# Kernel optimization log

Hardware: AMD Instinct MI355X
Metric: run time of the kernel (lower is better)

Reference implementation:

```python
import jax, jax.numpy as jnp
import numpy as np

S, B, HID = 2048, 1, 2048
NH, HD = 16, 128  # heads, head_dim (kv_channels); NH*HD == HID
EPS = 1e-5


def setup_inputs() -> dict:
    key = jax.random.key(0)
    ks = jax.random.split(key, 5)
    sc_h = 1.0 / np.sqrt(HID)
    return {
        "hidden_states": jax.random.normal(ks[0], (S, B, HID), jnp.float32),
        "ln_weight": jnp.ones((HID,), jnp.float32),
        "ln_bias": jnp.zeros((HID,), jnp.float32),
        "qkv_weight": jax.random.normal(ks[1], (3 * HID, HID), jnp.float32) * sc_h,
        "qkv_bias": jax.random.normal(ks[2], (3 * HID,), jnp.float32) * 0.02,
        "proj_weight": jax.random.normal(ks[3], (HID, HID), jnp.float32) * sc_h,
        "proj_bias": jax.random.normal(ks[4], (HID,), jnp.float32) * 0.02,
    }


def reference(hidden_states, ln_weight, ln_bias, qkv_weight, qkv_bias, proj_weight, proj_bias):
    s, b, hid = hidden_states.shape
    # LayerNormLinear: LN over last dim, then fused QKV projection
    mu = jnp.mean(hidden_states, axis=-1, keepdims=True)
    var = jnp.mean(jnp.square(hidden_states - mu), axis=-1, keepdims=True)
    ln_x = (hidden_states - mu) * jax.lax.rsqrt(var + EPS) * ln_weight + ln_bias
    mixed = jnp.einsum('sbh,oh->sbo', ln_x, qkv_weight) + qkv_bias  # [S,B,3*HID]
    # fuse_qkv_params=False -> non-interleaved: reshape to [S,B,3*NH,HD], split on dim -2
    mixed = mixed.reshape(s, b, 3 * NH, HD)
    q, k, v = jnp.split(mixed, 3, axis=2)  # each [S,B,NH,HD]
    # scaled dot-product attention with causal mask
    scale = 1.0 / np.sqrt(HD)
    scores = jnp.einsum('sbhd,tbhd->bhst', q, k) * scale  # [B,NH,S,S]
    causal = jnp.tril(jnp.ones((s, s), bool))
    scores = jnp.where(causal, scores, -jnp.inf)
    probs = jax.nn.softmax(scores, axis=-1)
    ctx = jnp.einsum('bhst,tbhd->sbhd', probs, v).reshape(s, b, hid)
    # output projection
    out = jnp.einsum('sbh,oh->sbo', ctx, proj_weight) + proj_bias
    return out
```

## Files before the change

### kernel.cpp

```cpp
#include <hip/hip_runtime.h>
#include <stdint.h>

#define S_LEN 2048
#define HID   2048
#define NHEAD 16
#define HDIM  128
#define LDQK  4096

typedef unsigned short ushort_t;
using bf16x8 = __attribute__((ext_vector_type(8))) short;
using f32x4  = __attribute__((ext_vector_type(4))) float;

__device__ __forceinline__ float bf2f(ushort_t u) {
  union { uint32_t i; float f; } v; v.i = ((uint32_t)u) << 16; return v.f;
}
__device__ __forceinline__ ushort_t f2bf(float f) {
  union { float f; uint32_t i; } v; v.f = f;
  uint32_t r = v.i + 0x7fffu + ((v.i >> 16) & 1u);
  return (ushort_t)(r >> 16);
}
__device__ __forceinline__ void store_val(ushort_t* C, size_t idx, float v) { C[idx] = f2bf(v); }
__device__ __forceinline__ void store_val(float* C, size_t idx, float v) { C[idx] = v; }

__device__ __forceinline__ bf16x8 load8(const ushort_t* p) { return *(const bf16x8*)p; }
__device__ __forceinline__ bf16x8 load8(const float* p) {
  float4 a = *(const float4*)p, b = *(const float4*)(p + 4);
  ushort_t o[8] = { f2bf(a.x), f2bf(a.y), f2bf(a.z), f2bf(a.w),
                    f2bf(b.x), f2bf(b.y), f2bf(b.z), f2bf(b.w) };
  return *(const bf16x8*)o;
}

__device__ __forceinline__ void gl_lds16(const ushort_t* g, short* l) {
  __builtin_amdgcn_global_load_lds((const __attribute__((address_space(1))) void*)g,
                                   (__attribute__((address_space(3))) void*)l, 16, 0, 0);
}

__global__ __launch_bounds__(256) void ln_cvt_fused(const float* __restrict__ x,
                                                    const float* __restrict__ w,
                                                    const float* __restrict__ bln,
                                                    ushort_t* __restrict__ y,
                                                    const float* __restrict__ s1,
                                                    ushort_t* __restrict__ d1, int n1,
                                                    const float* __restrict__ s2,
                                                    ushort_t* __restrict__ d2, int n2) {
  const int t = threadIdx.x;
  if ((int)blockIdx.x >= S_LEN) {
    int i = ((int)blockIdx.x - S_LEN) * 256 + t;
    const float* src; ushort_t* dst;
    if (i < n1) { src = s1; dst = d1; }
    else { i -= n1; if (i >= n2) return; src = s2; dst = d2; }
    float4 a = ((const float4*)src)[i * 2], c = ((const float4*)src)[i * 2 + 1];
    ushort_t o[8] = { f2bf(a.x), f2bf(a.y), f2bf(a.z), f2bf(a.w),
                      f2bf(c.x), f2bf(c.y), f2bf(c.z), f2bf(c.w) };
    ((uint4*)dst)[i] = *(const uint4*)o;
    return;
  }
  const int row = blockIdx.x;
  const float4* xr = (const float4*)(x + (size_t)row * HID);
  float4 v0 = xr[t], v1 = xr[t + 256];
  float s  = v0.x + v0.y + v0.z + v0.w + v1.x + v1.y + v1.z + v1.w;
  float ss = v0.x*v0.x + v0.y*v0.y + v0.z*v0.z + v0.w*v0.w
           + v1.x*v1.x + v1.y*v1.y + v1.z*v1.z + v1.w*v1.w;
#pragma unroll
  for (int off = 32; off > 0; off >>= 1) { s += __shfl_xor(s, off, 64); ss += __shfl_xor(ss, off, 64); }
  __shared__ float red[8];
  const int wv = t >> 6;
  if ((t & 63) == 0) { red[wv * 2] = s; red[wv * 2 + 1] = ss; }
  __syncthreads();
  s  = red[0] + red[2] + red[4] + red[6];
  ss = red[1] + red[3] + red[5] + red[7];
  const float mu   = s * (1.f / HID);
  const float var  = ss * (1.f / HID) - mu * mu;
  const float rstd = rsqrtf(var + 1e-5f);
  const float4* wr = (const float4*)w;
  const float4* br = (const float4*)bln;
  float4 w0 = wr[t], w1 = wr[t + 256];
  float4 b0 = br[t], b1 = br[t + 256];
  ushort_t* yr = y + (size_t)row * HID;
  ushort_t o0[4] = { f2bf((v0.x - mu) * rstd * w0.x + b0.x), f2bf((v0.y - mu) * rstd * w0.y + b0.y),
                     f2bf((v0.z - mu) * rstd * w0.z + b0.z), f2bf((v0.w - mu) * rstd * w0.w + b0.w) };
  ushort_t o1[4] = { f2bf((v1.x - mu) * rstd * w1.x + b1.x), f2bf((v1.y - mu) * rstd * w1.y + b1.y),
                     f2bf((v1.z - mu) * rstd * w1.z + b1.z), f2bf((v1.w - mu) * rstd * w1.w + b1.w) };
  *(uint2*)(&yr[4 * t])         = *(const uint2*)o0;
  *(uint2*)(&yr[4 * (t + 256)]) = *(const uint2*)o1;
}

__global__ __launch_bounds__(256) void ln_kernel(const float* __restrict__ x,
                                                 const float* __restrict__ w,
                                                 const float* __restrict__ b,
                                                 ushort_t* __restrict__ y) {
  const int row = blockIdx.x;
  const int t = threadIdx.x;
  const float4* xr = (const float4*)(x + (size_t)row * HID);
  float4 v0 = xr[t], v1 = xr[t + 256];
  float s  = v0.x + v0.y + v0.z + v0.w + v1.x + v1.y + v1.z + v1.w;
  float ss = v0.x*v0.x + v0.y*v0.y + v0.z*v0.z + v0.w*v0.w
           + v1.x*v1.x + v1.y*v1.y + v1.z*v1.z + v1.w*v1.w;
#pragma unroll
  for (int off = 32; off > 0; off >>= 1) { s += __shfl_xor(s, off, 64); ss += __shfl_xor(ss, off, 64); }
  __shared__ float red[8];
  const int wv = t >> 6;
  if ((t & 63) == 0) { red[wv * 2] = s; red[wv * 2 + 1] = ss; }
  __syncthreads();
  s  = red[0] + red[2] + red[4] + red[6];
  ss = red[1] + red[3] + red[5] + red[7];
  const float mu   = s * (1.f / HID);
  const float var  = ss * (1.f / HID) - mu * mu;
  const float rstd = rsqrtf(var + 1e-5f);
  const float4* wr = (const float4*)w;
  const float4* br = (const float4*)b;
  float4 w0 = wr[t], w1 = wr[t + 256];
  float4 b0 = br[t], b1 = br[t + 256];
  ushort_t* yr = y + (size_t)row * HID;
  ushort_t o0[4] = { f2bf((v0.x - mu) * rstd * w0.x + b0.x), f2bf((v0.y - mu) * rstd * w0.y + b0.y),
                     f2bf((v0.z - mu) * rstd * w0.z + b0.z), f2bf((v0.w - mu) * rstd * w0.w + b0.w) };
  ushort_t o1[4] = { f2bf((v1.x - mu) * rstd * w1.x + b1.x), f2bf((v1.y - mu) * rstd * w1.y + b1.y),
                     f2bf((v1.z - mu) * rstd * w1.z + b1.z), f2bf((v1.w - mu) * rstd * w1.w + b1.w) };
  *(uint2*)(&yr[4 * t])         = *(const uint2*)o0;
  *(uint2*)(&yr[4 * (t + 256)]) = *(const uint2*)o1;
}

template <int MT, bool SPLIT, typename OUT_T>
__global__ __launch_bounds__(256, 3) void gemm_lds(const ushort_t* __restrict__ A,
                                                   const ushort_t* __restrict__ B,
                                                   const float* __restrict__ bias,
                                                   OUT_T* __restrict__ C,
                                                   ushort_t* __restrict__ VTg,
                                                   int M, int N, int K, int ldc) {
  constexpr int MI = MT / 32;
  __shared__ __align__(16) short As[2][MT * 32];
  __shared__ __align__(16) short Bs[2][128 * 32];
  const int mb = blockIdx.x * MT, nb = blockIdx.y * 128;
  const int t = threadIdx.x, wave = t >> 6, lane = t & 63;
  const int wm = (wave >> 1) * (MT / 2), wn = (wave & 1) * 64;
  const int lrow = lane & 15, quad = lane >> 4;
  const int srow = lane >> 2, scol = (lane & 3) * 8;
  const f32x4 vzero = {0.f, 0.f, 0.f, 0.f};

  f32x4 acc[MI][4];
#pragma unroll
  for (int i = 0; i < MI; i++)
#pragma unroll
    for (int j = 0; j < 4; j++) acc[i][j] = vzero;

  auto stage = [&](int k0, int buf) {
#pragma unroll
    for (int kb = 0; kb < MT / 64; kb++) {
      const int c = wave * (MT / 64) + kb;
      gl_lds16(&A[(size_t)(mb + c * 16 + srow) * K + k0 + scol], &As[buf][c * 512]);
    }
#pragma unroll
    for (int kb = 0; kb < 2; kb++) {
      const int c = wave * 2 + kb;
      gl_lds16(&B[(size_t)(nb + c * 16 + srow) * K + k0 + scol], &Bs[buf][c * 512]);
    }
  };

  stage(0, 0);
  int cur = 0;
  for (int k0 = 0; k0 < K; k0 += 32) {
    __syncthreads();
    if (k0 + 32 < K) stage(k0 + 32, cur ^ 1);
    bf16x8 af[MI], bfg[4];
#pragma unroll
    for (int mi = 0; mi < MI; mi++) af[mi] = *(const bf16x8*)(&As[cur][(wm + mi * 16 + lrow) * 32 + quad * 8]);
#pragma unroll
    for (int ni = 0; ni < 4; ni++) bfg[ni] = *(const bf16x8*)(&Bs[cur][(wn + ni * 16 + lrow) * 32 + quad * 8]);
#pragma unroll
    for (int mi = 0; mi < MI; mi++)
#pragma unroll
      for (int ni = 0; ni < 4; ni++)
        acc[mi][ni] = __builtin_amdgcn_mfma_f32_16x16x32_bf16(af[mi], bfg[ni], acc[mi][ni], 0, 0, 0);
    cur ^= 1;
  }

#pragma unroll
  for (int mi = 0; mi < MI; mi++)
#pragma unroll
    for (int ni = 0; ni < 4; ni++) {
      const int col = nb + wn + ni * 16 + lrow;
      const float bv = bias[col];
      const int row0 = mb + wm + mi * 16 + quad * 4;
      if (SPLIT && col >= 4096) {
        ushort_t o4[4];
#pragma unroll
        for (int r = 0; r < 4; r++) o4[r] = f2bf(acc[mi][ni][r] + bv);
        *(uint2*)(&VTg[(size_t)(col - 4096) * S_LEN + row0]) = *(const uint2*)o4;
      } else {
#pragma unroll
        for (int r = 0; r < 4; r++)
          store_val(C, (size_t)(row0 + r) * ldc + col, acc[mi][ni][r] + bv);
      }
    }
}

template <bool SPLIT, typename OUT_T, typename BT>
__global__ __launch_bounds__(256, 3) void gemm_bt(const ushort_t* __restrict__ A,
                                                  const BT* __restrict__ B,
                                                  const float* __restrict__ bias,
                                                  OUT_T* __restrict__ C,
                                                  ushort_t* __restrict__ VTg,
                                                  int M, int N, int K, int ldc) {
  __shared__ __align__(16) short As[128 * 40];
  __shared__ __align__(16) short Bs[128 * 40];
  const int mb = blockIdx.x * 128, nb = blockIdx.y * 128;
  const int t = threadIdx.x, wave = t >> 6, lane = t & 63;
  const int wm = (wave >> 1) * 64, wn = (wave & 1) * 64;
  const int lrow = lane & 15, quad = lane >> 4;
  const f32x4 vzero = {0.f, 0.f, 0.f, 0.f};
  f32x4 acc[4][4];
#pragma unroll
  for (int i = 0; i < 4; i++)
#pragma unroll
    for (int j = 0; j < 4; j++) acc[i][j] = vzero;
  for (int k0 = 0; k0 < K; k0 += 32) {
    __syncthreads();
#pragma unroll
    for (int i = 0; i < 2; i++) {
      int c = t + 256 * i;
      int r = c >> 2, kc = (c & 3) * 8;
      *(bf16x8*)(&As[r * 40 + kc]) = load8(&A[(size_t)(mb + r) * K + k0 + kc]);
      *(bf16x8*)(&Bs[r * 40 + kc]) = load8(&B[(size_t)(nb + r) * K + k0 + kc]);
    }
    __syncthreads();
    bf16x8 af[4], bfg[4];
#pragma unroll
    for (int mi = 0; mi < 4; mi++) af[mi] = *(const bf16x8*)(&As[(wm + mi * 16 + lrow) * 40 + quad * 8]);
#pragma unroll
    for (int ni = 0; ni < 4; ni++) bfg[ni] = *(const bf16x8*)(&Bs[(wn + ni * 16 + lrow) * 40 + quad * 8]);
#pragma unroll
    for (int mi = 0; mi < 4; mi++)
#pragma unroll
      for (int ni = 0; ni < 4; ni++)
        acc[mi][ni] = __builtin_amdgcn_mfma_f32_16x16x32_bf16(af[mi], bfg[ni], acc[mi][ni], 0, 0, 0);
  }
#pragma unroll
  for (int mi = 0; mi < 4; mi++)
#pragma unroll
    for (int ni = 0; ni < 4; ni++) {
      const int col = nb + wn + ni * 16 + lrow;
      const float bv = bias[col];
      const int row0 = mb + wm + mi * 16 + quad * 4;
      if (SPLIT && col >= 4096) {
        ushort_t o4[4];
#pragma unroll
        for (int r = 0; r < 4; r++) o4[r] = f2bf(acc[mi][ni][r] + bv);
        *(uint2*)(&VTg[(size_t)(col - 4096) * S_LEN + row0]) = *(const uint2*)o4;
      } else {
#pragma unroll
        for (int r = 0; r < 4; r++)
          store_val(C, (size_t)(row0 + r) * ldc + col, acc[mi][ni][r] + bv);
      }
    }
}

__global__ __launch_bounds__(256, 2) void attn_kernel(const ushort_t* __restrict__ mixedQK,
                                                      const ushort_t* __restrict__ vtg,
                                                      ushort_t* __restrict__ ctx) {
  const int bid = blockIdx.x;
  const int xcd = bid & 7;
  const int slot = bid >> 3;
  const int h = xcd * 2 + (slot & 1);
  const int qi = slot >> 1;
  const int qblk = (qi < 16) ? (31 - qi) : (qi - 16);
  const int t = threadIdx.x;
  const int wave = t >> 6, lane = t & 63;
  const int lrow = lane & 15, quad = lane >> 4;
  const float scale = 0.08838834764831845f;
  const float SHIFT = 8.0f;

  __shared__ __align__(16) short Ks[64 * 128];
  __shared__ __align__(16) short VTs[2][128 * 64];
  __shared__ __align__(16) short Ps[4][16 * 72];

  const int krow_off = wave * 4 + (lane >> 4);
  const int kgrp = (lane & 15) ^ krow_off;
  const int vrow_off = wave * 8 + (lane >> 3);
  const int vgrp = (lane & 7) ^ (lane >> 3);
  const ushort_t* Kbase = mixedQK + 2048 + h * HDIM;
  const ushort_t* Vbase = vtg + (size_t)h * HDIM * S_LEN;

  const f32x4 vzero = {0.f, 0.f, 0.f, 0.f};

  auto stageK = [&](int kv0) {
#pragma unroll
    for (int i = 0; i < 4; i++)
      gl_lds16(Kbase + (size_t)(kv0 + i * 16 + krow_off) * LDQK + kgrp * 8,
               &Ks[(i * 256 + wave * 64) * 8]);
  };
  auto stageV = [&](int kv0, int buf) {
#pragma unroll
    for (int i = 0; i < 4; i++)
      gl_lds16(Vbase + (size_t)(i * 32 + vrow_off) * S_LEN + kv0 + vgrp * 8,
               &VTs[buf][(i * 256 + wave * 64) * 8]);
  };

  stageK(0);
  stageV(0, 0);

  const int ntiles = qblk + 1;
  const int q0 = qblk * 64 + wave * 16;

  bf16x8 qf[4];
  {
    const ushort_t* Qb = mixedQK + (size_t)(q0 + lrow) * LDQK + h * HDIM;
#pragma unroll
    for (int c = 0; c < 4; c++) qf[c] = *(const bf16x8*)(Qb + c * 32 + quad * 8);
  }

  float lsum[4] = {0.f, 0.f, 0.f, 0.f};
  f32x4 acc[8];
#pragma unroll
  for (int d = 0; d < 8; d++) acc[d] = vzero;

  for (int tk = 0; tk < ntiles; ++tk) {
    const int kv0 = tk * 64;
    __syncthreads();
    if (tk + 1 < ntiles) stageV((tk + 1) * 64, (tk + 1) & 1);

    f32x4 sc[4];
#pragma unroll
    for (int ni = 0; ni < 4; ni++) sc[ni] = vzero;
    __builtin_amdgcn_s_setprio(1);
#pragma unroll
    for (int ni = 0; ni < 4; ni++)
#pragma unroll
      for (int c = 0; c < 4; c++) {
        bf16x8 kf = *(const bf16x8*)(&Ks[(((ni * 16 + lrow) << 4) + ((c * 4 + quad) ^ lrow)) * 8]);
        sc[ni] = __builtin_amdgcn_mfma_f32_16x16x32_bf16(qf[c], kf, sc[ni], 0, 0, 0);
      }
    __builtin_amdgcn_s_setprio(0);

    asm volatile("s_waitcnt lgkmcnt(0)\n\ts_barrier" ::: "memory");
    if (tk + 1 < ntiles) stageK((tk + 1) * 64);

    short* P = &Ps[wave][0];
#pragma unroll
    for (int r = 0; r < 4; r++) {
      const int row = q0 + quad * 4 + r;
#pragma unroll
      for (int ni = 0; ni < 4; ni++) {
        const int col = kv0 + ni * 16 + lrow;
        float pe = (col > row) ? 0.f : __expf(sc[ni][r] * scale - SHIFT);
        lsum[r] += pe;
        P[(quad * 4 + r) * 72 + ni * 16 + lrow] = (short)f2bf(pe);
      }
    }

    bf16x8 pf[2];
#pragma unroll
    for (int c = 0; c < 2; c++) pf[c] = *(const bf16x8*)(&P[lrow * 72 + c * 32 + quad * 8]);

    const short* Vc = VTs[tk & 1];
    __builtin_amdgcn_s_setprio(1);
#pragma unroll
    for (int d = 0; d < 8; d++)
#pragma unroll
      for (int c = 0; c < 2; c++) {
        bf16x8 vf = *(const bf16x8*)(&Vc[(((d * 16 + lrow) << 3) + ((c * 4 + quad) ^ (lrow & 7))) * 8]);
        acc[d] = __builtin_amdgcn_mfma_f32_16x16x32_bf16(pf[c], vf, acc[d], 0, 0, 0);
      }
    __builtin_amdgcn_s_setprio(0);
  }

  float inv_l[4];
#pragma unroll
  for (int r = 0; r < 4; r++) {
    float l = lsum[r];
#pragma unroll
    for (int off = 1; off < 16; off <<= 1) l += __shfl_xor(l, off, 16);
    inv_l[r] = 1.f / l;
  }
#pragma unroll
  for (int d = 0; d < 8; d++)
#pragma unroll
    for (int r = 0; r < 4; r++) {
      const int row = q0 + quad * 4 + r;
      ctx[(size_t)row * HID + h * HDIM + d * 16 + lrow] = f2bf(acc[d][r] * inv_l[r]);
    }
}

extern "C" void kernel_launch(void* const* d_in, const int* in_sizes, int n_in,
                              void* d_out, int out_size, void* d_ws, size_t ws_size,
                              hipStream_t stream) {
  const float* hidden = (const float*)d_in[0];
  const float* lnw    = (const float*)d_in[1];
  const float* lnb    = (const float*)d_in[2];
  const float* qkvw   = (const float*)d_in[3];
  const float* qkvb   = (const float*)d_in[4];
  const float* projw  = (const float*)d_in[5];
  const float* projb  = (const float*)d_in[6];
  float* out = (float*)d_out;

  char* ws = (char*)d_ws;
  ushort_t* ln_x    = (ushort_t*)ws;
  ushort_t* mixedQK = (ushort_t*)(ws + ((size_t)8 << 20));
  ushort_t* vtg     = (ushort_t*)(ws + ((size_t)24 << 20));
  ushort_t* qkvw_bf = (ushort_t*)(ws + ((size_t)32 << 20));
  ushort_t* projw_bf= (ushort_t*)(ws + ((size_t)56 << 20));
  ushort_t* ctxb    = ln_x;
  const bool big = ws_size >= ((size_t)64 << 20);

  if (big) {
    ln_cvt_fused<<<S_LEN + 8192, 256, 0, stream>>>(
        hidden, lnw, lnb, ln_x,
        qkvw, qkvw_bf, 3 * HID * HID / 8,
        projw, projw_bf, HID * HID / 8);
    gemm_lds<128, true, ushort_t><<<dim3(16, 48), 256, 0, stream>>>(
        ln_x, qkvw_bf, qkvb, mixedQK, vtg, S_LEN, 3 * HID, HID, LDQK);
  } else {
    ln_kernel<<<S_LEN, 256, 0, stream>>>(hidden, lnw, lnb, ln_x);
    gemm_bt<true, ushort_t, float><<<dim3(16, 48), 256, 0, stream>>>(
        ln_x, qkvw, qkvb, mixedQK, vtg, S_LEN, 3 * HID, HID, LDQK);
  }
  attn_kernel<<<512, 256, 0, stream>>>(mixedQK, vtg, ctxb);
  if (big) {
    gemm_lds<64, false, float><<<dim3(32, 16), 256, 0, stream>>>(
        ctxb, projw_bf, projb, out, nullptr, S_LEN, HID, HID, HID);
  } else {
    gemm_bt<false, float, float><<<dim3(16, 16), 256, 0, stream>>>(
        ctxb, projw, projb, out, nullptr, S_LEN, HID, HID, HID);
  }
}
```

Before: 264.6 us.

## Split-K the output projection GEMM into two halves plus reduction kernel

After: 265.0 us, median of 3. No clear change (+0.2%).

```diff
diff --git a/kernel.cpp b/kernel.cpp
--- a/kernel.cpp
+++ b/kernel.cpp
@@ -194,6 +194,80 @@
     }
 }
 
+__global__ __launch_bounds__(256, 3) void gemm_proj_sk(const ushort_t* __restrict__ A,
+                                                       const ushort_t* __restrict__ B,
+                                                       const float* __restrict__ bias,
+                                                       float* __restrict__ C,
+                                                       float* __restrict__ Ctmp,
+                                                       int M, int N, int K, int ldc) {
+  __shared__ __align__(16) short As[2][128 * 32];
+  __shared__ __align__(16) short Bs[2][128 * 32];
+  const int mb = blockIdx.x * 128, nb = blockIdx.y * 128;
+  const int z = blockIdx.z;
+  const int kbase = z * (K >> 1), KH = K >> 1;
+  const int t = threadIdx.x, wave = t >> 6, lane = t & 63;
+  const int wm = (wave >> 1) * 64, wn = (wave & 1) * 64;
+  const int lrow = lane & 15, quad = lane >> 4;
+  const int srow = lane >> 2, scol = (lane & 3) * 8;
+  const f32x4 vzero = {0.f, 0.f, 0.f, 0.f};
+
+  f32x4 acc[4][4];
+#pragma unroll
+  for (int i = 0; i < 4; i++)
+#pragma unroll
+    for (int j = 0; j < 4; j++) acc[i][j] = vzero;
+
+  auto stage = [&](int k0, int buf) {
+#pragma unroll
+    for (int kb = 0; kb < 2; kb++) {
+      const int c = wave * 2 + kb;
+      gl_lds16(&A[(size_t)(mb + c * 16 + srow) * K + kbase + k0 + scol], &As[buf][c * 512]);
+      gl_lds16(&B[(size_t)(nb + c * 16 + srow) * K + kbase + k0 + scol], &Bs[buf][c * 512]);
+    }
+  };
+
+  stage(0, 0);
+  int cur = 0;
+  for (int k0 = 0; k0 < KH; k0 += 32) {
+    __syncthreads();
+    if (k0 + 32 < KH) stage(k0 + 32, cur ^ 1);
+    bf16x8 af[4], bfg[4];
+#pragma unroll
+    for (int mi = 0; mi < 4; mi++) af[mi] = *(const bf16x8*)(&As[cur][(wm + mi * 16 + lrow) * 32 + quad * 8]);
+#pragma unroll
+    for (int ni = 0; ni < 4; ni++) bfg[ni] = *(const bf16x8*)(&Bs[cur][(wn + ni * 16 + lrow) * 32 + quad * 8]);
+#pragma unroll
+    for (int mi = 0; mi < 4; mi++)
+#pragma unroll
+      for (int ni = 0; ni < 4; ni++)
+        acc[mi][ni] = __builtin_amdgcn_mfma_f32_16x16x32_bf16(af[mi], bfg[ni], acc[mi][ni], 0, 0, 0);
+    cur ^= 1;
+  }
+
+  float* dst = z ? Ctmp : C;
+#pragma unroll
+  for (int mi = 0; mi < 4; mi++)
+#pragma unroll
+    for (int ni = 0; ni < 4; ni++) {
+      const int col = nb + wn + ni * 16 + lrow;
+      const float bv = z ? 0.f : bias[col];
+      const int row0 = mb + wm + mi * 16 + quad * 4;
+#pragma unroll
+      for (int r = 0; r < 4; r++)
+        dst[(size_t)(row0 + r) * ldc + col] = acc[mi][ni][r] + bv;
+    }
+}
+
+__global__ __launch_bounds__(256) void add_f32(float* __restrict__ dst,
+                                               const float* __restrict__ src, int n4) {
+  int i = blockIdx.x * 256 + threadIdx.x;
+  if (i >= n4) return;
+  float4 a = ((const float4*)dst)[i];
+  float4 b = ((const float4*)src)[i];
+  a.x += b.x; a.y += b.y; a.z += b.z; a.w += b.w;
+  ((float4*)dst)[i] = a;
+}
+
 template <bool SPLIT, typename OUT_T, typename BT>
 __global__ __launch_bounds__(256, 3) void gemm_bt(const ushort_t* __restrict__ A,
                                                   const BT* __restrict__ B,
@@ -398,6 +472,7 @@
   ushort_t* vtg     = (ushort_t*)(ws + ((size_t)24 << 20));
   ushort_t* qkvw_bf = (ushort_t*)(ws + ((size_t)32 << 20));
   ushort_t* projw_bf= (ushort_t*)(ws + ((size_t)56 << 20));
+  float*    proj_tmp= (float*)(ws + ((size_t)8 << 20));
   ushort_t* ctxb    = ln_x;
   const bool big = ws_size >= ((size_t)64 << 20);
 
@@ -415,8 +490,9 @@
   }
   attn_kernel<<<512, 256, 0, stream>>>(mixedQK, vtg, ctxb);
   if (big) {
-    gemm_lds<64, false, float><<<dim3(32, 16), 256, 0, stream>>>(
-        ctxb, projw_bf, projb, out, nullptr, S_LEN, HID, HID, HID);
+    gemm_proj_sk<<<dim3(16, 16, 2), 256, 0, stream>>>(
+        ctxb, projw_bf, projb, out, proj_tmp, S_LEN, HID, HID, HID);
+    add_f32<<<4096, 256, 0, stream>>>(out, proj_tmp, S_LEN * HID / 4);
   } else {
     gemm_bt<false, float, float><<<dim3(16, 16), 256, 0, stream>>>(
         ctxb, projw, projb, out, nullptr, S_LEN, HID, HID, HID);
```
